# Optimization experiments

Measured on AMD Instinct MI355X. Metric: run time of the kernel, lower is better.

The kernel has to match this reference:

```python
import jax, jax.numpy as jnp
import numpy as np
import math

N, DIM, HEADS = 4096, 128, 8
HC = DIM // HEADS      # MHA per-head dim = 16
GC = DIM               # TransformerConv per-head out_channels = dim (concat=False)
E = 65536
FFN = 2048
EPS = 1e-5

def layernorm(x, g, b):
    m = x.mean(-1, keepdims=True)
    v = ((x - m) ** 2).mean(-1, keepdims=True)
    return (x - m) * jax.lax.rsqrt(v + EPS) * g + b

def setup_inputs() -> dict:
    key = jax.random.key(0)
    ks = jax.random.split(key, 24)
    s = 0.02
    def nrm(k, shape):
        return jax.random.normal(k, shape, jnp.float32) * s
    return dict(
        x=jax.random.normal(ks[0], (N, DIM), jnp.float32),
        edge_index=jax.random.randint(ks[1], (2, E), 0, N),
        edge_attr=jax.random.normal(ks[2], (E, DIM), jnp.float32),
        n1_g=jnp.ones((DIM,)), n1_b=jnp.zeros((DIM,)),
        n2_g=jnp.ones((DIM,)), n2_b=jnp.zeros((DIM,)),
        n3_g=jnp.ones((DIM,)), n3_b=jnp.zeros((DIM,)),
        w_qkv=nrm(ks[3], (DIM, 3 * DIM)), b_qkv=jnp.zeros((3 * DIM,)),
        w_o=nrm(ks[4], (DIM, DIM)), b_o=jnp.zeros((DIM,)),
        w_query=nrm(ks[5], (DIM, HEADS * GC)), b_query=jnp.zeros((HEADS * GC,)),
        w_key=nrm(ks[6], (DIM, HEADS * GC)), b_key=jnp.zeros((HEADS * GC,)),
        w_value=nrm(ks[7], (DIM, HEADS * GC)), b_value=jnp.zeros((HEADS * GC,)),
        w_edge=nrm(ks[8], (DIM, HEADS * GC)), b_edge=jnp.zeros((HEADS * GC,)),
        w_skip=nrm(ks[9], (DIM, GC)), b_skip=jnp.zeros((GC,)),
        w_beta=nrm(ks[10], (3 * GC, 1)),
        w_f1=nrm(ks[11], (DIM, FFN)), b_f1=jnp.zeros((FFN,)),
        w_f2=nrm(ks[12], (FFN, DIM)), b_f2=jnp.zeros((DIM,)),
        w_dyn=nrm(ks[13], (2 * DIM, DIM)), b_dyn=jnp.zeros((DIM,)),
    )

def reference(x, edge_index, edge_attr, n1_g, n1_b, n2_g, n2_b, n3_g, n3_b,
              w_qkv, b_qkv, w_o, b_o,
              w_query, b_query, w_key, b_key, w_value, b_value,
              w_edge, b_edge, w_skip, b_skip, w_beta,
              w_f1, b_f1, w_f2, b_f2, w_dyn, b_dyn):
    residual = x
    xn = layernorm(x, n1_g, n1_b)
    # ---- dense self-attention (batch 1, batch_first MHA, eval mode) ----
    qkv = xn @ w_qkv + b_qkv
    q, k, v = jnp.split(qkv, 3, axis=-1)
    q = q.reshape(N, HEADS, HC)
    k = k.reshape(N, HEADS, HC)
    v = v.reshape(N, HEADS, HC)
    scores = jnp.einsum('qhd,khd->hqk', q, k) / math.sqrt(HC)
    probs = jax.nn.softmax(scores, axis=-1)
    attn = jnp.einsum('hqk,khd->qhd', probs, v).reshape(N, DIM)
    attn = attn @ w_o + b_o
    x = residual + attn
    # ---- TransformerConv (heads=8, concat=False -> mean, beta=True, edge_dim=dim) ----
    xn2 = layernorm(x, n2_g, n2_b)
    src, dst = edge_index[0], edge_index[1]   # source -> target flow
    qg = (xn2 @ w_query + b_query).reshape(N, HEADS, GC)
    kg = (xn2 @ w_key + b_key).reshape(N, HEADS, GC)
    vg = (xn2 @ w_value + b_value).reshape(N, HEADS, GC)
    eg = (edge_attr @ w_edge + b_edge).reshape(E, HEADS, GC)
    kj = kg[src] + eg                          # key_j + edge embedding
    alpha = jnp.einsum('ehd,ehd->eh', qg[dst], kj) / math.sqrt(GC)  # [E,H]
    amax = jax.ops.segment_max(alpha, dst, num_segments=N)          # [N,H]
    amax = jnp.where(jnp.isfinite(amax), amax, 0.0)
    ea = jnp.exp(alpha - amax[dst])
    denom = jax.ops.segment_sum(ea, dst, num_segments=N)
    w = ea / (denom[dst] + 1e-16)              # segment softmax per target node
    msg = (vg[src] + eg) * w[:, :, None]       # value_j + edge, scaled
    agg = jax.ops.segment_sum(msg, dst, num_segments=N)  # [N,H,GC]
    out = agg.mean(axis=1)                     # concat=False -> head mean
    x_r = xn2 @ w_skip + b_skip                # root/skip path
    beta = jax.nn.sigmoid(jnp.concatenate([out, x_r, out - x_r], axis=-1) @ w_beta)
    graph_out = beta * x_r + (1.0 - beta) * out
    x = x + graph_out
    # ---- FFN ----
    xn3 = layernorm(x, n3_g, n3_b)
    ffn = jax.nn.gelu(xn3 @ w_f1 + b_f1, approximate=False) @ w_f2 + b_f2
    x = x + ffn
    # ---- gated residual fusion ----
    gate = jax.nn.sigmoid(jnp.concatenate([x, residual], axis=-1) @ w_dyn + b_dyn)
    return x * gate + residual * (1.0 - gate)
```

## Files before the change

kernel.cpp:

```cpp
#include <hip/hip_runtime.h>
#include <math.h>
#include <cstddef>

#define NN 4096
#define DIMC 128
#define NHEADS 8
#define NE 65536

typedef unsigned short ushort_t;
typedef short bs8 __attribute__((ext_vector_type(8)));
typedef float f32x16 __attribute__((ext_vector_type(16)));
typedef _Float16 h4 __attribute__((ext_vector_type(4)));
typedef float f4t __attribute__((ext_vector_type(4)));

__device__ __forceinline__ float b2f(ushort_t u){
  unsigned int i = ((unsigned int)u)<<16; float f;
  __builtin_memcpy(&f,&i,4); return f;
}
__device__ __forceinline__ ushort_t f2b(float f){
  unsigned int x; __builtin_memcpy(&x,&f,4);
  unsigned int r = x + 0x7fffu + ((x>>16)&1u);
  return (ushort_t)(r>>16);
}
__device__ __forceinline__ float bdot8(uint4 a, uint4 b){
  unsigned int ua[4]={a.x,a.y,a.z,a.w}, ub[4]={b.x,b.y,b.z,b.w};
  float s=0.f;
  #pragma unroll
  for (int i=0;i<4;++i){
    unsigned int al=ua[i]<<16, ah=ua[i]&0xffff0000u, bl=ub[i]<<16, bh=ub[i]&0xffff0000u;
    float fa,fb,fc,fd;
    __builtin_memcpy(&fa,&al,4); __builtin_memcpy(&fb,&ah,4);
    __builtin_memcpy(&fc,&bl,4); __builtin_memcpy(&fd,&bh,4);
    s += fa*fc + fb*fd;
  }
  return s;
}
__device__ __forceinline__ float bfdot8(uint4 a, const float* __restrict__ e){
  unsigned int ua[4]={a.x,a.y,a.z,a.w};
  float s=0.f;
  #pragma unroll
  for (int i=0;i<4;++i){
    unsigned int al=ua[i]<<16, ah=ua[i]&0xffff0000u;
    float fa,fb;
    __builtin_memcpy(&fa,&al,4); __builtin_memcpy(&fb,&ah,4);
    s += fa*e[2*i] + fb*e[2*i+1];
  }
  return s;
}

__global__ __launch_bounds__(128) void ln_kernel(const float* __restrict__ x,
    const float* __restrict__ g, const float* __restrict__ b, ushort_t* __restrict__ y){
  int n = blockIdx.x, d = threadIdx.x;
  __shared__ float red[128];
  float v = x[(size_t)n*DIMC + d];
  red[d] = v; __syncthreads();
  for (int off=64; off>0; off>>=1){ if (d<off) red[d]+=red[d+off]; __syncthreads(); }
  float mean = red[0]*(1.0f/128.0f);
  __syncthreads();
  float c = v-mean;
  red[d] = c*c; __syncthreads();
  for (int off=64; off>0; off>>=1){ if (d<off) red[d]+=red[d+off]; __syncthreads(); }
  float var = red[0]*(1.0f/128.0f);
  y[(size_t)n*DIMC+d] = f2b(c*rsqrtf(var+1e-5f)*g[d]+b[d]);
}

__global__ __launch_bounds__(256) void megawcvt_kernel(
    const float* __restrict__ w_qkv, const float* __restrict__ w_o,
    const float* __restrict__ w_q, const float* __restrict__ w_k,
    const float* __restrict__ w_v, const float* __restrict__ w_s,
    const float* __restrict__ w_e, const float* __restrict__ w_f1, const float* __restrict__ w_f2,
    const float* __restrict__ bq, const float* __restrict__ bk,
    const float* __restrict__ bv, const float* __restrict__ bs,
    const float* __restrict__ w_dyn,
    ushort_t* __restrict__ WBqkv, ushort_t* __restrict__ WBo, ushort_t* __restrict__ WBG,
    ushort_t* __restrict__ WETB, ushort_t* __restrict__ WBf1, ushort_t* __restrict__ WBf2,
    ushort_t* __restrict__ WEB8, float* __restrict__ BCAT, ushort_t* __restrict__ WDYN,
    int* __restrict__ COUNT)
{
  for (int id = blockIdx.x*256+threadIdx.x; id < 1301632; id += gridDim.x*256){
    if (id < 1261568){
      float v; ushort_t* dst; int local;
      if (id < 49152){ local=id; int n=local>>7,k=local&127; v=w_qkv[(size_t)k*384+n]; dst=&WBqkv[local]; }
      else if (id < 65536){ local=id-49152; int n=local>>7,k=local&127; v=w_o[(size_t)k*128+n]; dst=&WBo[local]; }
      else if (id < 475136){ local=id-65536; int n=local>>7,k=local&127;
        if (n<1024) v=w_q[(size_t)k*1024+n];
        else if (n<2048) v=w_k[(size_t)k*1024+n-1024];
        else if (n<3072) v=w_v[(size_t)k*1024+n-2048];
        else v=w_s[(size_t)k*128+n-3072];
        dst=&WBG[local]; }
      else if (id < 606208){ local=id-475136; int n=local>>7,k=local&127; v=w_e[(size_t)k*1024+n]; dst=&WETB[local]; }
      else if (id < 868352){ local=id-606208; int n=local>>7,k=local&127; v=w_f1[(size_t)k*2048+n]; dst=&WBf1[local]; }
      else if (id < 1130496){ local=id-868352; int n=local>>11,k=local&2047; v=w_f2[(size_t)k*128+n]; dst=&WBf2[local]; }
      else { local=id-1130496; int d=local>>10,kk=local&1023,hh=kk>>7,i2=kk&127;
        v=w_e[(size_t)i2*1024+hh*128+d]*0.125f; dst=&WEB8[local]; }
      *dst = f2b(v);
    } else if (id < 1264768){
      int local = id - 1261568;
      float v;
      if (local<1024) v=bq[local]; else if (local<2048) v=bk[local-1024];
      else if (local<3072) v=bv[local-2048]; else v=bs[local-3072];
      BCAT[local]=v;
    } else if (id < 1297536){
      int local = id - 1264768;
      WDYN[local] = f2b(w_dyn[local]);
    } else {
      COUNT[id-1297536]=0;
    }
  }
}

template<int A_BF16, int C_MODE>
__global__ __launch_bounds__(256) void mgemm_kernel(
    const void* __restrict__ Av, int lda, int strideA,
    const ushort_t* __restrict__ BT, int ldbt, int strideB,
    const float* __restrict__ bias,
    const float* __restrict__ res,
    void* __restrict__ Cv, int ldc, int strideC,
    int K, int act_gelu)
{
  int z = blockIdx.z;
  int m0 = blockIdx.y*128, n0 = blockIdx.x*64;
  int tid = threadIdx.x;
  int w = tid>>6, lane = tid&63;
  int kg = lane>>5;
  int ml = w*32 + (lane&31);
  int sw = (ml>>1)&3;
  __shared__ ushort_t As[128*32];
  const ushort_t* BTz = BT + (size_t)z*strideB;
  f32x16 acc[2];
  #pragma unroll
  for (int i=0;i<16;++i){ acc[0][i]=0.f; acc[1][i]=0.f; }

  for (int k0=0; k0<K; k0+=32){
    {
      int rr = tid>>1, kc = (tid&1)*16;
      int rowg = m0 + rr;
      ushort_t tmp[16] __attribute__((aligned(16)));
      if (A_BF16){
        const ushort_t* A = (const ushort_t*)Av + (size_t)z*strideA;
        uint4 u0 = *(const uint4*)&A[(size_t)rowg*lda + k0 + kc];
        uint4 u1 = *(const uint4*)&A[(size_t)rowg*lda + k0 + kc + 8];
        __builtin_memcpy(tmp, &u0, 16); __builtin_memcpy(tmp+8, &u1, 16);
      } else {
        const float* A = (const float*)Av + (size_t)z*strideA;
        const float* p = &A[(size_t)rowg*lda + k0 + kc];
        float4 f0=*(const float4*)p, f1=*(const float4*)(p+4);
        float4 f2v=*(const float4*)(p+8), f3=*(const float4*)(p+12);
        tmp[0]=f2b(f0.x); tmp[1]=f2b(f0.y); tmp[2]=f2b(f0.z); tmp[3]=f2b(f0.w);
        tmp[4]=f2b(f1.x); tmp[5]=f2b(f1.y); tmp[6]=f2b(f1.z); tmp[7]=f2b(f1.w);
        tmp[8]=f2b(f2v.x); tmp[9]=f2b(f2v.y); tmp[10]=f2b(f2v.z); tmp[11]=f2b(f2v.w);
        tmp[12]=f2b(f3.x); tmp[13]=f2b(f3.y); tmp[14]=f2b(f3.z); tmp[15]=f2b(f3.w);
      }
      int swr = (rr>>1)&3, c0 = kc>>3;
      *(uint4*)&As[rr*32 + (((c0  )^swr)*8)] = *(const uint4*)tmp;
      *(uint4*)&As[rr*32 + (((c0+1)^swr)*8)] = *(const uint4*)(tmp+8);
    }
    __syncthreads();
    bs8 a0 = *(bs8*)&As[ml*32 + (((0*2+kg)^sw)*8)];
    bs8 a1 = *(bs8*)&As[ml*32 + (((1*2+kg)^sw)*8)];
    #pragma unroll
    for (int nt=0; nt<2; ++nt){
      const ushort_t* bp = &BTz[(size_t)(n0 + nt*32 + (lane&31))*ldbt + k0 + kg*8];
      uint4 rb0 = *(const uint4*)bp;
      uint4 rb1 = *(const uint4*)(bp + 16);
      bs8 b0, b1;
      __builtin_memcpy(&b0, &rb0, 16); __builtin_memcpy(&b1, &rb1, 16);
      acc[nt] = __builtin_amdgcn_mfma_f32_32x32x16_bf16(a0, b0, acc[nt], 0,0,0);
      acc[nt] = __builtin_amdgcn_mfma_f32_32x32x16_bf16(a1, b1, acc[nt], 0,0,0);
    }
    __syncthreads();
  }
  #pragma unroll
  for (int nt=0; nt<2; ++nt){
    int col = n0 + nt*32 + (lane&31);
    float bv = bias ? bias[col] : 0.f;
    #pragma unroll
    for (int r=0; r<16; ++r){
      int rowl = (r&3) + 8*(r>>2) + 4*kg;
      int row = m0 + w*32 + rowl;
      float v = acc[nt][r] + bv;
      if (act_gelu) v = 0.5f*v*(1.0f+erff(v*0.70710678118654752f));
      if (res) v += res[(size_t)row*ldc + col];
      size_t idx = (size_t)z*strideC + (size_t)row*ldc + col;
      if (C_MODE==1)      ((ushort_t*)Cv)[idx] = f2b(v);
      else if (C_MODE==2) ((_Float16*)Cv)[idx] = (_Float16)v;
      else                ((float*)Cv)[idx]    = v;
    }
  }
}

__global__ __launch_bounds__(256) void vtrans_kernel(const _Float16* __restrict__ qkvh,
    _Float16* __restrict__ vt){
  int id = blockIdx.x*256+threadIdx.x;
  int n = id & 4095, d = id >> 12;
  vt[(size_t)d*4096 + n] = qkvh[(size_t)n*384 + 256 + d];
}

__global__ __launch_bounds__(256) void flash_kernel(const _Float16* __restrict__ qkvh,
    const _Float16* __restrict__ vt, float* __restrict__ attn){
  int h = blockIdx.y;
  int w = threadIdx.x >> 6, lane = threadIdx.x & 63;
  int q0 = blockIdx.x*64;
  int col = lane & 15, quad = lane >> 4;
  __shared__ float ll[4][4][16];
  __shared__ float lo[4][4][256];
  h4 qf[4];
  #pragma unroll
  for (int t=0;t<4;++t)
    qf[t] = *(const h4*)&qkvh[(size_t)(q0+t*16+col)*384 + h*16 + quad*4];
  f4t ov[4];
  float ls[4] = {0.f,0.f,0.f,0.f};
  #pragma unroll
  for (int t=0;t<4;++t){ ov[t][0]=0.f; ov[t][1]=0.f; ov[t][2]=0.f; ov[t][3]=0.f; }
  const _Float16* kbase = qkvh + 128 + h*16 + quad*4;
  const _Float16* vbase = vt + (size_t)(h*16+col)*4096 + quad*4;
  int jbeg = w*1024, jend = jbeg + 1024;
  h4 kf = *(const h4*)&kbase[(size_t)(jbeg+col)*384];
  h4 vf = *(const h4*)&vbase[jbeg];
  for (int j0=jbeg; j0<jend; j0+=16){
    h4 kc=kf, vc=vf;
    if (j0+16<jend){
      kf = *(const h4*)&kbase[(size_t)(j0+16+col)*384];
      vf = *(const h4*)&vbase[j0+16];
    }
    f4t s[4];
    #pragma unroll
    for (int t=0;t<4;++t){
      s[t][0]=0.f; s[t][1]=0.f; s[t][2]=0.f; s[t][3]=0.f;
      s[t] = __builtin_amdgcn_mfma_f32_16x16x16f16(kc, qf[t], s[t], 0,0,0);
    }
    #pragma unroll
    for (int t=0;t<4;++t){
      float p0=__expf(s[t][0]*0.25f), p1=__expf(s[t][1]*0.25f);
      float p2=__expf(s[t][2]*0.25f), p3=__expf(s[t][3]*0.25f);
      ls[t] += p0+p1+p2+p3;
      h4 pf; pf[0]=(_Float16)p0; pf[1]=(_Float16)p1; pf[2]=(_Float16)p2; pf[3]=(_Float16)p3;
      ov[t] = __builtin_amdgcn_mfma_f32_16x16x16f16(vc, pf, ov[t], 0,0,0);
    }
  }
  #pragma unroll
  for (int t=0;t<4;++t){
    float l = ls[t];
    l += __shfl_xor(l,16);
    l += __shfl_xor(l,32);
    if (lane<16) ll[w][t][lane]=l;
    *(float4*)&lo[w][t][lane*4] = make_float4(ov[t][0],ov[t][1],ov[t][2],ov[t][3]);
  }
  __syncthreads();
  {
    int t = w;
    float l = ll[0][t][col]+ll[1][t][col]+ll[2][t][col]+ll[3][t][col];
    float4 os = make_float4(0.f,0.f,0.f,0.f);
    #pragma unroll
    for (int ww=0; ww<4; ++ww){
      float4 owv = *(const float4*)&lo[ww][t][lane*4];
      os.x += owv.x; os.y += owv.y; os.z += owv.z; os.w += owv.w;
    }
    float inv = 1.0f/l;
    *(float4*)&attn[(size_t)(q0+t*16+col)*128 + h*16 + quad*4] =
        make_float4(os.x*inv, os.y*inv, os.z*inv, os.w*inv);
  }
}

__global__ __launch_bounds__(256) void alpha_kernel(const int* __restrict__ ei,
    const float* __restrict__ ea, const ushort_t* __restrict__ qkvsg,
    const ushort_t* __restrict__ t, const float* __restrict__ b_edge,
    const int* __restrict__ csr, float* __restrict__ alpha){
  int tid = threadIdx.x;
  int i = blockIdx.x*4 + (tid>>6);
  int lane = tid&63;
  int h = lane>>3, li = lane&7;
  int e = csr[i] & (NE-1);
  int src = ei[e] & (NN-1), dst = ei[NE+e] & (NN-1);
  int off = h*128 + li*16;
  uint4 q0v = *(const uint4*)&qkvsg[(size_t)dst*3200 + off];
  uint4 q1v = *(const uint4*)&qkvsg[(size_t)dst*3200 + off + 8];
  uint4 k0v = *(const uint4*)&qkvsg[(size_t)src*3200 + 1024 + off];
  uint4 k1v = *(const uint4*)&qkvsg[(size_t)src*3200 + 1024 + off + 8];
  uint4 t0v = *(const uint4*)&t[(size_t)dst*1024 + off];
  uint4 t1v = *(const uint4*)&t[(size_t)dst*1024 + off + 8];
  const float* ep = &ea[(size_t)e*128 + li*16];
  const float* bp = &b_edge[off];
  float p = bdot8(q0v,k0v) + bdot8(q1v,k1v)
          + bfdot8(t0v, ep) + bfdot8(t1v, ep+8)
          + bfdot8(q0v, bp) + bfdot8(q1v, bp+8);
  p += __shfl_xor(p,1); p += __shfl_xor(p,2); p += __shfl_xor(p,4);
  if (li==0)
    alpha[(size_t)e*8 + h] = 0.08838834764831845f*p;
}

__global__ __launch_bounds__(256) void count_kernel(const int* __restrict__ ei, int* __restrict__ cnt){
  int e = blockIdx.x*256+threadIdx.x;
  atomicAdd(&cnt[ei[NE+e] & (NN-1)],1);
}
__global__ __launch_bounds__(1024) void scan_kernel(const int* __restrict__ cnt,
    int* __restrict__ rows, int* __restrict__ cursor){
  __shared__ int sums[1024];
  int tid=threadIdx.x;
  int c0=cnt[tid*4], c1=cnt[tid*4+1], c2=cnt[tid*4+2], c3=cnt[tid*4+3];
  int local=c0+c1+c2+c3;
  sums[tid]=local;
  __syncthreads();
  for (int off=1; off<1024; off<<=1){
    int v = (tid>=off)? sums[tid-off] : 0;
    __syncthreads();
    sums[tid]+=v;
    __syncthreads();
  }
  int r = sums[tid]-local;
  rows[tid*4]=r;   cursor[tid*4]=r;   r+=c0;
  rows[tid*4+1]=r; cursor[tid*4+1]=r; r+=c1;
  rows[tid*4+2]=r; cursor[tid*4+2]=r; r+=c2;
  rows[tid*4+3]=r; cursor[tid*4+3]=r; r+=c3;
  if (tid==1023) rows[4096]=r;
}
__global__ __launch_bounds__(256) void scatter_kernel(const int* __restrict__ ei,
    int* __restrict__ cursor, int* __restrict__ csr){
  int e = blockIdx.x*256+threadIdx.x;
  int pos = atomicAdd(&cursor[ei[NE+e] & (NN-1)],1);
  if (pos >= 0 && pos < NE) csr[pos]=e;
}

__global__ __launch_bounds__(256) void agg1_kernel(
    const int* __restrict__ ei, const ushort_t* __restrict__ qkvsg, const float* __restrict__ ea,
    const float* __restrict__ abuf, const int* __restrict__ rows, const int* __restrict__ csr,
    const float* __restrict__ b_edge,
    ushort_t* __restrict__ eagg, float* __restrict__ part)
{
  int n = blockIdx.x, tid = threadIdx.x;
  int d = tid & 127, h0 = tid >> 7;
  float racc[4]={0.f,0.f,0.f,0.f}, eacc[4]={0.f,0.f,0.f,0.f}, wsacc[4]={0.f,0.f,0.f,0.f};
  float mh[4]={-1e30f,-1e30f,-1e30f,-1e30f}, den[4]={0.f,0.f,0.f,0.f};
  float be[4];
  #pragma unroll
  for (int j=0;j<4;++j) be[j] = b_edge[(h0+2*j)*128 + d];
  int i0=rows[n], i1=rows[n+1];
  i0 = max(0,min(i0,NE)); i1 = max(i0,min(i1,NE));
  for (int i=i0;i<i1;++i){
    int e = csr[i]&(NE-1);
    #pragma unroll
    for (int j=0;j<4;++j) mh[j] = fmaxf(mh[j], abuf[(size_t)e*8 + h0 + 2*j]);
  }
  for (int i=i0;i<i1;++i){
    int e = csr[i]&(NE-1);
    int sr = ei[e]&(NN-1);
    float eav = ea[(size_t)e*128 + d];
    const ushort_t* vgp = &qkvsg[(size_t)sr*3200 + 2048];
    #pragma unroll
    for (int j=0;j<4;++j){
      float wv = __expf(abuf[(size_t)e*8 + h0 + 2*j] - mh[j]);
      den[j] += wv;
      racc[j] += wv * b2f(vgp[tid + j*256]);
      eacc[j] += wv * eav;
      wsacc[j] += wv;
    }
  }
  float partial = 0.f;
  #pragma unroll
  for (int j=0;j<4;++j){
    float inv = 1.0f/(den[j]+1e-16f);
    eagg[(size_t)n*1024 + tid + j*256] = f2b(eacc[j]*inv);
    partial += (racc[j] + wsacc[j]*be[j])*inv;
  }
  __shared__ float pp[2][128];
  pp[h0][d] = partial;
  __syncthreads();
  if (tid<128) part[(size_t)n*128+tid] = (pp[0][tid]+pp[1][tid])*0.125f;
}

__global__ __launch_bounds__(128) void combine_kernel(float* __restrict__ x2,
    const float* __restrict__ corrp, int nz, const float* __restrict__ part,
    const ushort_t* __restrict__ qkvsg, const float* __restrict__ x1,
    const float* __restrict__ w_beta)
{
  int n=blockIdx.x, d=threadIdx.x;
  __shared__ float sred[128];
  __shared__ float sbeta;
  size_t idx = (size_t)n*128+d;
  float o = part[idx];
  for (int z=0; z<nz; ++z) o += corrp[(size_t)z*524288 + idx];
  float xrv = b2f(qkvsg[(size_t)n*3200 + 3072 + d]);
  sred[d] = o*w_beta[d] + xrv*w_beta[128+d] + (o-xrv)*w_beta[256+d];
  __syncthreads();
  for (int off=64; off>0; off>>=1){ if (d<off) sred[d]+=sred[d+off]; __syncthreads(); }
  if (d==0) sbeta = 1.0f/(1.0f+__expf(-sred[0]));
  __syncthreads();
  float beta=sbeta;
  x2[idx] = x1[idx] + beta*xrv + (1.0f-beta)*o;
}

__global__ __launch_bounds__(128) void gate_kernel(const float* __restrict__ x3p,
    const float* __restrict__ b_f2, const float* __restrict__ x2,
    const float* __restrict__ x0, const ushort_t* __restrict__ wdyn,
    const float* __restrict__ b_dyn, float* __restrict__ out){
  int n=blockIdx.x, d=threadIdx.x;
  __shared__ float s[256];
  size_t idx = (size_t)n*128+d;
  float a = x3p[idx] + x3p[524288+idx] + x3p[1048576+idx] + x3p[1572864+idx]
          + b_f2[d] + x2[idx];
  float r = x0[idx];
  s[d]=a; s[128+d]=r;
  __syncthreads();
  float g = b_dyn[d];
  for (int k=0;k<256;++k) g += s[k]*b2f(wdyn[(size_t)k*128+d]);
  g = 1.0f/(1.0f+__expf(-g));
  out[idx] = a*g + r*(1.0f-g);
}

extern "C" void kernel_launch(void* const* d_in, const int* in_sizes, int n_in,
                              void* d_out, int out_size, void* d_ws, size_t ws_size,
                              hipStream_t stream) {
  const float* x    =(const float*)d_in[0];
  const int*   ei   =(const int*)  d_in[1];
  const float* eattr=(const float*)d_in[2];
  const float* n1g=(const float*)d_in[3], *n1b=(const float*)d_in[4];
  const float* n2g=(const float*)d_in[5], *n2b=(const float*)d_in[6];
  const float* n3g=(const float*)d_in[7], *n3b=(const float*)d_in[8];
  const float* w_qkv=(const float*)d_in[9],  *b_qkv=(const float*)d_in[10];
  const float* w_o  =(const float*)d_in[11], *b_o  =(const float*)d_in[12];
  const float* w_q  =(const float*)d_in[13], *b_q  =(const float*)d_in[14];
  const float* w_k  =(const float*)d_in[15], *b_k  =(const float*)d_in[16];
  const float* w_v  =(const float*)d_in[17], *b_v  =(const float*)d_in[18];
  const float* w_e  =(const float*)d_in[19], *b_e  =(const float*)d_in[20];
  const float* w_s  =(const float*)d_in[21], *b_s  =(const float*)d_in[22];
  const float* w_beta=(const float*)d_in[23];
  const float* w_f1 =(const float*)d_in[24], *b_f1=(const float*)d_in[25];
  const float* w_f2 =(const float*)d_in[26], *b_f2=(const float*)d_in[27];
  const float* w_dyn=(const float*)d_in[28], *b_dyn=(const float*)d_in[29];
  float* out=(float*)d_out;
  float* ws=(float*)d_ws;

  float* X1    = ws + 0;
  float* X2    = ws + 524288;
  ushort_t* LNS = (ushort_t*)(ws + 1048576);
  float* ALPHA = ws + 1572864;
  int*   ROWS  = (int*)(ws + 2129920);
  int*   CURS  = (int*)(ws + 2134080);
  int*   CSR   = (int*)(ws + 2138176);
  int*   COUNT = (int*)(ws + 2203712);
  ushort_t* WBqkv = (ushort_t*)(ws + 2207808);
  ushort_t* WBo   = (ushort_t*)(ws + 2232384);
  ushort_t* WBG   = (ushort_t*)(ws + 2240576);
  ushort_t* WETB  = (ushort_t*)(ws + 2445376);
  ushort_t* WBf1  = (ushort_t*)(ws + 2510912);
  ushort_t* WBf2  = (ushort_t*)(ws + 2641984);
  ushort_t* WEB8  = (ushort_t*)(ws + 2773056);
  float* BCAT  = ws + 2838592;
  ushort_t* WDYN = (ushort_t*)(ws + 2841792);
  _Float16* QKVH  = (_Float16*)(ws + 2858176);
  _Float16* VT    = (_Float16*)(ws + 3644608);
  ushort_t* QKVSG = (ushort_t*)(ws + 2858176);
  ushort_t* T     = (ushort_t*)(ws + 9411776);
  ushort_t* EAGG  = (ushort_t*)(ws + 9411776);
  ushort_t* MID   = (ushort_t*)(ws + 2858176);
  float* X3P   = ws + 9411776;
  float* ATTN  = X2;
  float* PART  = ws + 1048576;

  int big = (ws_size >= (size_t)13605952*4) ? 1 : 0;
  float* CORRP = big ? (ws + 11508928) : ALPHA;
  int nz = big ? 4 : 1;

  megawcvt_kernel<<<2048,256,0,stream>>>(w_qkv,w_o,w_q,w_k,w_v,w_s,w_e,w_f1,w_f2,
                                         b_q,b_k,b_v,b_s,w_dyn,
                                         WBqkv,WBo,WBG,WETB,WBf1,WBf2,WEB8,BCAT,WDYN,COUNT);

  ln_kernel<<<NN,128,0,stream>>>(x, n1g, n1b, LNS);
  mgemm_kernel<1,2><<<dim3(6,32,1),256,0,stream>>>(LNS,128,0, WBqkv,128,0, b_qkv, nullptr, QKVH,384,0, 128, 0);
  vtrans_kernel<<<2048,256,0,stream>>>(QKVH, VT);
  flash_kernel<<<dim3(64,8),256,0,stream>>>(QKVH, VT, ATTN);
  mgemm_kernel<0,0><<<dim3(2,32,1),256,0,stream>>>(ATTN,128,0, WBo,128,0, b_o, x, X1,128,0, 128, 0);

  ln_kernel<<<NN,128,0,stream>>>(X1, n2g, n2b, LNS);
  mgemm_kernel<1,1><<<dim3(50,32,1),256,0,stream>>>(LNS,128,0, WBG,128,0, BCAT, nullptr, QKVSG,3200,0, 128, 0);
  mgemm_kernel<1,1><<<dim3(2,32,8),256,0,stream>>>(QKVSG,3200,128, WETB,128,16384, nullptr, nullptr, T,1024,128, 128, 0);
  count_kernel<<<256,256,0,stream>>>(ei, COUNT);
  scan_kernel<<<1,1024,0,stream>>>(COUNT, ROWS, CURS);
  scatter_kernel<<<256,256,0,stream>>>(ei, CURS, CSR);
  alpha_kernel<<<16384,256,0,stream>>>(ei, eattr, QKVSG, T, b_e, CSR, ALPHA);
  agg1_kernel<<<NN,256,0,stream>>>(ei, QKVSG, eattr, ALPHA, ROWS, CSR, b_e, EAGG, PART);
  if (big)
    mgemm_kernel<1,0><<<dim3(2,32,4),256,0,stream>>>(EAGG,1024,256, WEB8,1024,256, nullptr, nullptr, CORRP,128,524288, 256, 0);
  else
    mgemm_kernel<1,0><<<dim3(2,32,1),256,0,stream>>>(EAGG,1024,0, WEB8,1024,0, nullptr, nullptr, CORRP,128,0, 1024, 0);
  combine_kernel<<<NN,128,0,stream>>>(X2, CORRP, nz, PART, QKVSG, X1, w_beta);

  ln_kernel<<<NN,128,0,stream>>>(X2, n3g, n3b, LNS);
  mgemm_kernel<1,1><<<dim3(32,32,1),256,0,stream>>>(LNS,128,0, WBf1,128,0, b_f1, nullptr, MID,2048,0, 128, 1);
  mgemm_kernel<1,0><<<dim3(2,32,4),256,0,stream>>>(MID,2048,512, WBf2,2048,512, nullptr, nullptr, X3P,128,524288, 512, 0);

  gate_kernel<<<NN,128,0,stream>>>(X3P, b_f2, X2, x, WDYN, b_dyn, out);
}
```

Before: 434.1 us.

## Aggregate layernormed inputs instead of projected values, apply value weights after aggregation

```diff
diff --git a/kernel.cpp b/kernel.cpp
--- a/kernel.cpp
+++ b/kernel.cpp
@@ -67,44 +67,40 @@
 __global__ __launch_bounds__(256) void megawcvt_kernel(
     const float* __restrict__ w_qkv, const float* __restrict__ w_o,
     const float* __restrict__ w_q, const float* __restrict__ w_k,
-    const float* __restrict__ w_v, const float* __restrict__ w_s,
-    const float* __restrict__ w_e, const float* __restrict__ w_f1, const float* __restrict__ w_f2,
+    const float* __restrict__ w_v, const float* __restrict__ w_e,
+    const float* __restrict__ w_f1, const float* __restrict__ w_f2,
     const float* __restrict__ bq, const float* __restrict__ bk,
-    const float* __restrict__ bv, const float* __restrict__ bs,
     const float* __restrict__ w_dyn,
     ushort_t* __restrict__ WBqkv, ushort_t* __restrict__ WBo, ushort_t* __restrict__ WBG,
     ushort_t* __restrict__ WETB, ushort_t* __restrict__ WBf1, ushort_t* __restrict__ WBf2,
-    ushort_t* __restrict__ WEB8, float* __restrict__ BCAT, ushort_t* __restrict__ WDYN,
+    ushort_t* __restrict__ WCAT, float* __restrict__ BCAT, ushort_t* __restrict__ WDYN,
     int* __restrict__ COUNT)
 {
-  for (int id = blockIdx.x*256+threadIdx.x; id < 1301632; id += gridDim.x*256){
-    if (id < 1261568){
+  for (int id = blockIdx.x*256+threadIdx.x; id < 1284096; id += gridDim.x*256){
+    if (id < 1245184){
       float v; ushort_t* dst; int local;
       if (id < 49152){ local=id; int n=local>>7,k=local&127; v=w_qkv[(size_t)k*384+n]; dst=&WBqkv[local]; }
       else if (id < 65536){ local=id-49152; int n=local>>7,k=local&127; v=w_o[(size_t)k*128+n]; dst=&WBo[local]; }
-      else if (id < 475136){ local=id-65536; int n=local>>7,k=local&127;
-        if (n<1024) v=w_q[(size_t)k*1024+n];
-        else if (n<2048) v=w_k[(size_t)k*1024+n-1024];
-        else if (n<3072) v=w_v[(size_t)k*1024+n-2048];
-        else v=w_s[(size_t)k*128+n-3072];
+      else if (id < 327680){ local=id-65536; int n=local>>7,k=local&127;
+        v = (n<1024) ? w_q[(size_t)k*1024+n] : w_k[(size_t)k*1024+n-1024];
         dst=&WBG[local]; }
-      else if (id < 606208){ local=id-475136; int n=local>>7,k=local&127; v=w_e[(size_t)k*1024+n]; dst=&WETB[local]; }
-      else if (id < 868352){ local=id-606208; int n=local>>7,k=local&127; v=w_f1[(size_t)k*2048+n]; dst=&WBf1[local]; }
-      else if (id < 1130496){ local=id-868352; int n=local>>11,k=local&2047; v=w_f2[(size_t)k*128+n]; dst=&WBf2[local]; }
-      else { local=id-1130496; int d=local>>10,kk=local&1023,hh=kk>>7,i2=kk&127;
-        v=w_e[(size_t)i2*1024+hh*128+d]*0.125f; dst=&WEB8[local]; }
+      else if (id < 458752){ local=id-327680; int n=local>>7,k=local&127; v=w_e[(size_t)k*1024+n]; dst=&WETB[local]; }
+      else if (id < 720896){ local=id-458752; int n=local>>7,k=local&127; v=w_f1[(size_t)k*2048+n]; dst=&WBf1[local]; }
+      else if (id < 983040){ local=id-720896; int n=local>>11,k=local&2047; v=w_f2[(size_t)k*128+n]; dst=&WBf2[local]; }
+      else { local=id-983040; int d=local>>11, k=local&2047;
+        int h=(k&1023)>>7, i=k&127;
+        const float* src = (k<1024) ? w_v : w_e;
+        v = src[(size_t)i*1024 + h*128 + d]*0.125f;
+        dst=&WCAT[local]; }
       *dst = f2b(v);
-    } else if (id < 1264768){
-      int local = id - 1261568;
-      float v;
-      if (local<1024) v=bq[local]; else if (local<2048) v=bk[local-1024];
-      else if (local<3072) v=bv[local-2048]; else v=bs[local-3072];
-      BCAT[local]=v;
-    } else if (id < 1297536){
-      int local = id - 1264768;
+    } else if (id < 1247232){
+      int local = id - 1245184;
+      BCAT[local] = (local<1024) ? bq[local] : bk[local-1024];
+    } else if (id < 1280000){
+      int local = id - 1247232;
       WDYN[local] = f2b(w_dyn[local]);
     } else {
-      COUNT[id-1297536]=0;
+      COUNT[id-1280000]=0;
     }
   }
 }
@@ -273,10 +269,10 @@
   int e = csr[i] & (NE-1);
   int src = ei[e] & (NN-1), dst = ei[NE+e] & (NN-1);
   int off = h*128 + li*16;
-  uint4 q0v = *(const uint4*)&qkvsg[(size_t)dst*3200 + off];
-  uint4 q1v = *(const uint4*)&qkvsg[(size_t)dst*3200 + off + 8];
-  uint4 k0v = *(const uint4*)&qkvsg[(size_t)src*3200 + 1024 + off];
-  uint4 k1v = *(const uint4*)&qkvsg[(size_t)src*3200 + 1024 + off + 8];
+  uint4 q0v = *(const uint4*)&qkvsg[(size_t)dst*2048 + off];
+  uint4 q1v = *(const uint4*)&qkvsg[(size_t)dst*2048 + off + 8];
+  uint4 k0v = *(const uint4*)&qkvsg[(size_t)src*2048 + 1024 + off];
+  uint4 k1v = *(const uint4*)&qkvsg[(size_t)src*2048 + 1024 + off + 8];
   uint4 t0v = *(const uint4*)&t[(size_t)dst*1024 + off];
   uint4 t1v = *(const uint4*)&t[(size_t)dst*1024 + off + 8];
   const float* ep = &ea[(size_t)e*128 + li*16];
@@ -322,18 +318,21 @@
 }
 
 __global__ __launch_bounds__(256) void agg1_kernel(
-    const int* __restrict__ ei, const ushort_t* __restrict__ qkvsg, const float* __restrict__ ea,
+    const int* __restrict__ ei, const ushort_t* __restrict__ lns, const float* __restrict__ ea,
     const float* __restrict__ abuf, const int* __restrict__ rows, const int* __restrict__ csr,
-    const float* __restrict__ b_edge,
-    ushort_t* __restrict__ eagg, float* __restrict__ part)
+    const float* __restrict__ b_edge, const float* __restrict__ b_v,
+    ushort_t* __restrict__ seagg, float* __restrict__ part)
 {
   int n = blockIdx.x, tid = threadIdx.x;
   int d = tid & 127, h0 = tid >> 7;
-  float racc[4]={0.f,0.f,0.f,0.f}, eacc[4]={0.f,0.f,0.f,0.f}, wsacc[4]={0.f,0.f,0.f,0.f};
-  float mh[4]={-1e30f,-1e30f,-1e30f,-1e30f}, den[4]={0.f,0.f,0.f,0.f};
+  float sacc[4]={0.f,0.f,0.f,0.f}, eacc[4]={0.f,0.f,0.f,0.f}, wsacc[4]={0.f,0.f,0.f,0.f};
+  float mh[4]={-1e30f,-1e30f,-1e30f,-1e30f};
   float be[4];
   #pragma unroll
-  for (int j=0;j<4;++j) be[j] = b_edge[(h0+2*j)*128 + d];
+  for (int j=0;j<4;++j){
+    int hd = (h0+2*j)*128 + d;
+    be[j] = b_edge[hd] + b_v[hd];
+  }
   int i0=rows[n], i1=rows[n+1];
   i0 = max(0,min(i0,NE)); i1 = max(i0,min(i1,NE));
   for (int i=i0;i<i1;++i){
@@ -341,26 +340,45 @@
     #pragma unroll
     for (int j=0;j<4;++j) mh[j] = fmaxf(mh[j], abuf[(size_t)e*8 + h0 + 2*j]);
   }
-  for (int i=i0;i<i1;++i){
-    int e = csr[i]&(NE-1);
-    int sr = ei[e]&(NN-1);
-    float eav = ea[(size_t)e*128 + d];
-    const ushort_t* vgp = &qkvsg[(size_t)sr*3200 + 2048];
-    #pragma unroll
-    for (int j=0;j<4;++j){
-      float wv = __expf(abuf[(size_t)e*8 + h0 + 2*j] - mh[j]);
-      den[j] += wv;
-      racc[j] += wv * b2f(vgp[tid + j*256]);
-      eacc[j] += wv * eav;
-      wsacc[j] += wv;
-    }
+  __shared__ float smh[8];
+  __shared__ float wls[16][8];
+  __shared__ int es[16], srcs[16];
+  if (d==0){
+    #pragma unroll
+    for (int j=0;j<4;++j) smh[h0+2*j]=mh[j];
+  }
+  __syncthreads();
+  for (int cs=i0; cs<i1; cs+=16){
+    int cnt = min(16, i1-cs);
+    if (tid < cnt){ int e=csr[cs+tid]&(NE-1); es[tid]=e; srcs[tid]=ei[e]&(NN-1); }
+    if (tid < cnt*8){
+      int k=tid>>3, hh=tid&7;
+      int e=csr[cs+k]&(NE-1);
+      wls[k][hh] = __expf(abuf[(size_t)e*8+hh]-smh[hh]);
+    }
+    __syncthreads();
+    for (int k=0;k<cnt;++k){
+      int e = es[k], sr = srcs[k];
+      float lv = b2f(lns[(size_t)sr*128 + d]);
+      float eav = ea[(size_t)e*128 + d];
+      #pragma unroll
+      for (int j=0;j<4;++j){
+        float wv = wls[k][h0+2*j];
+        sacc[j] += wv*lv;
+        eacc[j] += wv*eav;
+        wsacc[j] += wv;
+      }
+    }
+    __syncthreads();
   }
   float partial = 0.f;
   #pragma unroll
   for (int j=0;j<4;++j){
-    float inv = 1.0f/(den[j]+1e-16f);
-    eagg[(size_t)n*1024 + tid + j*256] = f2b(eacc[j]*inv);
-    partial += (racc[j] + wsacc[j]*be[j])*inv;
+    float inv = 1.0f/(wsacc[j]+1e-16f);
+    int hd = (h0+2*j)*128 + d;
+    seagg[(size_t)n*2048 + hd]        = f2b(sacc[j]*inv);
+    seagg[(size_t)n*2048 + 1024 + hd] = f2b(eacc[j]*inv);
+    partial += be[j]*wsacc[j]*inv;
   }
   __shared__ float pp[2][128];
   pp[h0][d] = partial;
@@ -369,17 +387,22 @@
 }
 
 __global__ __launch_bounds__(128) void combine_kernel(float* __restrict__ x2,
-    const float* __restrict__ corrp, int nz, const float* __restrict__ part,
-    const ushort_t* __restrict__ qkvsg, const float* __restrict__ x1,
+    const float* __restrict__ corrp, const float* __restrict__ part,
+    const ushort_t* __restrict__ lns, const float* __restrict__ w_s,
+    const float* __restrict__ b_s, const float* __restrict__ x1,
     const float* __restrict__ w_beta)
 {
   int n=blockIdx.x, d=threadIdx.x;
+  __shared__ float lnrow[128];
   __shared__ float sred[128];
   __shared__ float sbeta;
   size_t idx = (size_t)n*128+d;
-  float o = part[idx];
-  for (int z=0; z<nz; ++z) o += corrp[(size_t)z*524288 + idx];
-  float xrv = b2f(qkvsg[(size_t)n*3200 + 3072 + d]);
+  lnrow[d] = b2f(lns[idx]);
+  __syncthreads();
+  float xrv = b_s[d];
+  #pragma unroll 4
+  for (int i=0;i<128;++i) xrv += lnrow[i]*w_s[(size_t)i*128+d];
+  float o = part[idx] + corrp[idx] + corrp[524288+idx] + corrp[1048576+idx] + corrp[1572864+idx];
   sred[d] = o*w_beta[d] + xrv*w_beta[128+d] + (o-xrv)*w_beta[256+d];
   __syncthreads();
   for (int off=64; off>0; off>>=1){ if (d<off) sred[d]+=sred[d+off]; __syncthreads(); }
@@ -433,37 +456,34 @@
   float* X1    = ws + 0;
   float* X2    = ws + 524288;
   ushort_t* LNS = (ushort_t*)(ws + 1048576);
-  float* ALPHA = ws + 1572864;
-  int*   ROWS  = (int*)(ws + 2129920);
-  int*   CURS  = (int*)(ws + 2134080);
-  int*   CSR   = (int*)(ws + 2138176);
-  int*   COUNT = (int*)(ws + 2203712);
-  ushort_t* WBqkv = (ushort_t*)(ws + 2207808);
-  ushort_t* WBo   = (ushort_t*)(ws + 2232384);
-  ushort_t* WBG   = (ushort_t*)(ws + 2240576);
-  ushort_t* WETB  = (ushort_t*)(ws + 2445376);
-  ushort_t* WBf1  = (ushort_t*)(ws + 2510912);
-  ushort_t* WBf2  = (ushort_t*)(ws + 2641984);
-  ushort_t* WEB8  = (ushort_t*)(ws + 2773056);
-  float* BCAT  = ws + 2838592;
-  ushort_t* WDYN = (ushort_t*)(ws + 2841792);
-  _Float16* QKVH  = (_Float16*)(ws + 2858176);
-  _Float16* VT    = (_Float16*)(ws + 3644608);
-  ushort_t* QKVSG = (ushort_t*)(ws + 2858176);
-  ushort_t* T     = (ushort_t*)(ws + 9411776);
-  ushort_t* EAGG  = (ushort_t*)(ws + 9411776);
-  ushort_t* MID   = (ushort_t*)(ws + 2858176);
-  float* X3P   = ws + 9411776;
+  float* PART  = ws + 1310720;
+  float* ALPHA = ws + 1835008;
+  int*   ROWS  = (int*)(ws + 2359296);
+  int*   CURS  = (int*)(ws + 2363456);
+  int*   CSR   = (int*)(ws + 2367552);
+  int*   COUNT = (int*)(ws + 2433088);
+  ushort_t* WBqkv = (ushort_t*)(ws + 2437184);
+  ushort_t* WBo   = (ushort_t*)(ws + 2461760);
+  ushort_t* WBG   = (ushort_t*)(ws + 2469952);
+  ushort_t* WETB  = (ushort_t*)(ws + 2601024);
+  ushort_t* WBf1  = (ushort_t*)(ws + 2666560);
+  ushort_t* WBf2  = (ushort_t*)(ws + 2797632);
+  ushort_t* WCAT  = (ushort_t*)(ws + 2928704);
+  float* BCAT  = ws + 3059776;
+  ushort_t* WDYN = (ushort_t*)(ws + 3061824);
+  _Float16* QKVH  = (_Float16*)(ws + 3078208);
+  _Float16* VT    = (_Float16*)(ws + 3864640);
+  ushort_t* QKVSG = (ushort_t*)(ws + 3078208);
+  ushort_t* SEAGG = (ushort_t*)(ws + 3078208);
+  ushort_t* MID   = (ushort_t*)(ws + 3078208);
+  ushort_t* T     = (ushort_t*)(ws + 7272512);
+  float* CORRP = ws + 7272512;
+  float* X3P   = ws + 7272512;
   float* ATTN  = X2;
-  float* PART  = ws + 1048576;
-
-  int big = (ws_size >= (size_t)13605952*4) ? 1 : 0;
-  float* CORRP = big ? (ws + 11508928) : ALPHA;
-  int nz = big ? 4 : 1;
-
-  megawcvt_kernel<<<2048,256,0,stream>>>(w_qkv,w_o,w_q,w_k,w_v,w_s,w_e,w_f1,w_f2,
-                                         b_q,b_k,b_v,b_s,w_dyn,
-                                         WBqkv,WBo,WBG,WETB,WBf1,WBf2,WEB8,BCAT,WDYN,COUNT);
+
+  megawcvt_kernel<<<2048,256,0,stream>>>(w_qkv,w_o,w_q,w_k,w_v,w_e,w_f1,w_f2,
+                                         b_q,b_k,w_dyn,
+                                         WBqkv,WBo,WBG,WETB,WBf1,WBf2,WCAT,BCAT,WDYN,COUNT);
 
   ln_kernel<<<NN,128,0,stream>>>(x, n1g, n1b, LNS);
   mgemm_kernel<1,2><<<dim3(6,32,1),256,0,stream>>>(LNS,128,0, WBqkv,128,0, b_qkv, nullptr, QKVH,384,0, 128, 0);
@@ -472,18 +492,15 @@
   mgemm_kernel<0,0><<<dim3(2,32,1),256,0,stream>>>(ATTN,128,0, WBo,128,0, b_o, x, X1,128,0, 128, 0);
 
   ln_kernel<<<NN,128,0,stream>>>(X1, n2g, n2b, LNS);
-  mgemm_kernel<1,1><<<dim3(50,32,1),256,0,stream>>>(LNS,128,0, WBG,128,0, BCAT, nullptr, QKVSG,3200,0, 128, 0);
-  mgemm_kernel<1,1><<<dim3(2,32,8),256,0,stream>>>(QKVSG,3200,128, WETB,128,16384, nullptr, nullptr, T,1024,128, 128, 0);
+  mgemm_kernel<1,1><<<dim3(32,32,1),256,0,stream>>>(LNS,128,0, WBG,128,0, BCAT, nullptr, QKVSG,2048,0, 128, 0);
+  mgemm_kernel<1,1><<<dim3(2,32,8),256,0,stream>>>(QKVSG,2048,128, WETB,128,16384, nullptr, nullptr, T,1024,128, 128, 0);
   count_kernel<<<256,256,0,stream>>>(ei, COUNT);
   scan_kernel<<<1,1024,0,stream>>>(COUNT, ROWS, CURS);
   scatter_kernel<<<256,256,0,stream>>>(ei, CURS, CSR);
   alpha_kernel<<<16384,256,0,stream>>>(ei, eattr, QKVSG, T, b_e, CSR, ALPHA);
-  agg1_kernel<<<NN,256,0,stream>>>(ei, QKVSG, eattr, ALPHA, ROWS, CSR, b_e, EAGG, PART);
-  if (big)
-    mgemm_kernel<1,0><<<dim3(2,32,4),256,0,stream>>>(EAGG,1024,256, WEB8,1024,256, nullptr, nullptr, CORRP,128,524288, 256, 0);
-  else
-    mgemm_kernel<1,0><<<dim3(2,32,1),256,0,stream>>>(EAGG,1024,0, WEB8,1024,0, nullptr, nullptr, CORRP,128,0, 1024, 0);
-  combine_kernel<<<NN,128,0,stream>>>(X2, CORRP, nz, PART, QKVSG, X1, w_beta);
+  agg1_kernel<<<NN,256,0,stream>>>(ei, LNS, eattr, ALPHA, ROWS, CSR, b_e, b_v, SEAGG, PART);
+  mgemm_kernel<1,0><<<dim3(2,32,4),256,0,stream>>>(SEAGG,2048,512, WCAT,2048,512, nullptr, nullptr, CORRP,128,524288, 512, 0);
+  combine_kernel<<<NN,128,0,stream>>>(X2, CORRP, PART, LNS, w_s, b_s, X1, w_beta);
 
   ln_kernel<<<NN,128,0,stream>>>(X2, n3g, n3b, LNS);
   mgemm_kernel<1,1><<<dim3(32,32,1),256,0,stream>>>(LNS,128,0, WBf1,128,0, b_f1, nullptr, MID,2048,0, 128, 1);
```

New measurement: 427.9 us. No clear change (-1.4%).
